# Kernel tuning notes

Hardware: AMD Instinct MI355X
Metric: run time of the kernel (lower is better)

The kernel has to match this reference:

```python
import jax, jax.numpy as jnp
import numpy as np

LRELU_ALPHA = 0.2
ACT_GAIN = float(np.sqrt(2.0))  # def_gain for 'lrelu' in StyleGAN2 bias_act


def setup_inputs() -> dict:
    key = jax.random.key(0)
    k_x, k_w, k_aw, k_wt = jax.random.split(key, 4)
    N, C_in, C_out, H, W, Wdim, K = 8, 256, 256, 128, 128, 512, 3
    x = jax.random.normal(k_x, (N, C_in, H, W), dtype=jnp.float32)
    w = jax.random.normal(k_w, (N, Wdim), dtype=jnp.float32)
    # FullyConnectedLayer params: weight ~ randn([out, in]) (lr_mult=1), bias_init=1
    affine_w = jax.random.normal(k_aw, (C_in, Wdim), dtype=jnp.float32)
    affine_b = jnp.ones((C_in,), dtype=jnp.float32)
    # Conv weight ~ randn, bias zeros
    weight = jax.random.normal(k_wt, (C_out, C_in, K, K), dtype=jnp.float32)
    bias = jnp.zeros((C_out,), dtype=jnp.float32)
    return {"x": x, "w": w, "affine_w": affine_w, "affine_b": affine_b,
            "weight": weight, "bias": bias}


def reference(x, w, affine_w, affine_b, weight, bias):
    N, C_in, H, W = x.shape
    C_out, _, K, _ = weight.shape
    # affine: runtime weight gain = 1/sqrt(in_features)
    wg = 1.0 / np.sqrt(affine_w.shape[1])
    styles = w @ (affine_w.T * wg) + affine_b                      # [N, C_in]
    # modulate: per-sample weights [N, C_out, C_in, K, K]
    ww = weight[None] * styles[:, None, :, None, None]
    # demodulate
    d = jax.lax.rsqrt(jnp.sum(ww * ww, axis=(2, 3, 4)) + 1e-8)     # [N, C_out]
    ww = ww * d[:, :, None, None, None]
    # fused per-sample conv via grouped conv (groups = N), flip_weight=True -> correlation
    x2 = x.reshape(1, N * C_in, H, W)
    wk = ww.reshape(N * C_out, C_in, K, K)
    pad = K // 2
    out = jax.lax.conv_general_dilated(
        x2, wk, window_strides=(1, 1), padding=((pad, pad), (pad, pad)),
        dimension_numbers=("NCHW", "OIHW", "NCHW"), feature_group_count=N)
    out = out.reshape(N, C_out, H, W)
    # bias_act: lrelu with def_gain sqrt(2), gain=1, no clamp; then sigmoid
    out = out + bias[None, :, None, None]
    out = jnp.where(out >= 0, out, LRELU_ALPHA * out) * ACT_GAIN
    return jax.nn.sigmoid(out)
```

## Files before the change

### kernel.cpp

```cpp
#include <hip/hip_runtime.h>
#include <hip/hip_bf16.h>

typedef __attribute__((ext_vector_type(8))) short bf16x8;
typedef __attribute__((ext_vector_type(4))) float f32x4;
typedef unsigned short ushort_t;

__device__ __forceinline__ void gload16(const void* g, void* l) {
  __builtin_amdgcn_global_load_lds(
      (const __attribute__((address_space(1))) void*)g,
      (__attribute__((address_space(3))) void*)l, 16, 0, 0);
}

__global__ void k_styles(const float* __restrict__ w, const float* __restrict__ aw,
                         const float* __restrict__ ab, float* __restrict__ styles) {
  int n = blockIdx.x;
  int ci = threadIdx.x;
  const float4* wr = (const float4*)(w + n * 512);
  const float4* ar = (const float4*)(aw + (size_t)ci * 512);
  float s = 0.f;
  #pragma unroll 4
  for (int j = 0; j < 128; j++) {
    float4 a = ar[j], b = wr[j];
    s += a.x * b.x + a.y * b.y + a.z * b.z + a.w * b.w;
  }
  styles[n * 256 + ci] = s * 0.044194173824159216f + ab[ci];
}

__global__ void k_modw(const float* __restrict__ weight, const float* __restrict__ styles,
                       ushort_t* __restrict__ wwg) {
  int id = blockIdx.x * 4 + (threadIdx.x >> 6);
  int l = threadIdx.x & 63;
  int n = id >> 8, co = id & 255;
  const float* wrow = weight + (size_t)co * 2304;
  const float* srow = styles + n * 256;
  float mv[36];
  float sum = 0.f;
  #pragma unroll
  for (int tap = 0; tap < 9; tap++) {
    #pragma unroll
    for (int cg = 0; cg < 4; cg++) {
      int ci = cg * 64 + l;
      float v = wrow[ci * 9 + tap] * srow[ci];
      mv[tap * 4 + cg] = v;
      sum += v * v;
    }
  }
  #pragma unroll
  for (int off = 32; off; off >>= 1) sum += __shfl_xor(sum, off, 64);
  float d = rsqrtf(sum + 1e-8f);
  #pragma unroll
  for (int tap = 0; tap < 9; tap++) {
    int kh = tap / 3, kw = tap % 3;
    #pragma unroll
    for (int cg = 0; cg < 4; cg++) {
      int ci = cg * 64 + l;
      float v = mv[tap * 4 + cg] * d;
      __hip_bfloat16 hb = __float2bfloat16(v);
      size_t oidx = ((((size_t)((n * 3 + kh) * 8) + (ci >> 5)) * 3 + kw) * 256 + co) * 32 + (ci & 31);
      wwg[oidx] = *reinterpret_cast<ushort_t*>(&hb);
    }
  }
}

__global__ void k_transpose(const float* __restrict__ x, ushort_t* __restrict__ xt) {
  int n = blockIdx.z, h = blockIdx.y;
  int wt = blockIdx.x & 1, ct = blockIdx.x >> 1;
  int w0 = wt * 64, ci0 = ct * 64;
  __shared__ float tile[64][65];
  int t = threadIdx.x;
  {
    int ci_l = t >> 2, wq = (t & 3) * 16;
    const float* src = x + (((size_t)(n * 256 + ci0 + ci_l) * 128 + h) * 128 + w0 + wq);
    #pragma unroll
    for (int j = 0; j < 4; j++) {
      float4 v = ((const float4*)src)[j];
      tile[ci_l][wq + j * 4 + 0] = v.x;
      tile[ci_l][wq + j * 4 + 1] = v.y;
      tile[ci_l][wq + j * 4 + 2] = v.z;
      tile[ci_l][wq + j * 4 + 3] = v.w;
    }
  }
  __syncthreads();
  {
    int w_l = t >> 2, cq = (t & 3) * 16;
    union { ushort_t u[16]; uint4 v[2]; } pk;
    #pragma unroll
    for (int j = 0; j < 16; j++) {
      __hip_bfloat16 hb = __float2bfloat16(tile[cq + j][w_l]);
      pk.u[j] = *reinterpret_cast<ushort_t*>(&hb);
    }
    size_t off = ((size_t)((n * 128 + h) * 128) + w0 + w_l) * 256 + ci0 + cq;
    uint4* dst = (uint4*)(xt + off);
    dst[0] = pk.v[0];
    dst[1] = pk.v[1];
  }
}

__global__ __launch_bounds__(256, 2) void k_conv(
    const ushort_t* __restrict__ xt, const ushort_t* __restrict__ wwg,
    const float* __restrict__ bias, float* __restrict__ out) {
  __shared__ __align__(16) char smem[24576 + 2 * 8448];
  char* sA = smem;
  char* sB = smem + 24576;

  const int cb = blockIdx.x;
  const int h0 = blockIdx.y * 2;
  const int n  = blockIdx.z;

  const int t = threadIdx.x;
  const int wave = t >> 6;
  const int l = t & 63;
  const int wr = wave >> 1, wc = wave & 1;
  const int c = l & 15, kg = l >> 4;

  f32x4 acc[4][8];
  #pragma unroll
  for (int i = 0; i < 4; i++)
    #pragma unroll
    for (int j = 0; j < 8; j++)
      acc[i][j] = (f32x4){0.f, 0.f, 0.f, 0.f};

  if (t < 64) {
    int buf = t >> 5;
    int r = t & 31;
    if (r < 16) {
      int rowsel = r >> 2;
      int row = (rowsel == 0) ? 0 : (128 + rowsel);
      *(f32x4*)(sB + buf * 8448 + row * 64 + (r & 3) * 16) = (f32x4){0.f, 0.f, 0.f, 0.f};
    }
  }

  const long long xtN = (long long)n * (128LL * 128 * 256);

  for (int kh = 0; kh < 3; kh++) {
    const int hsrc_w = h0 + wc + kh - 1;
    const bool valid = (hsrc_w >= 0) && (hsrc_w < 128);
    const char* gAkh = (const char*)(wwg + ((size_t)(n * 3 + kh)) * (8 * 3 * 256 * 32));
    for (int cc = 0; cc < 8; cc++) {
      __syncthreads();
      const char* gA = gAkh + (size_t)cc * (3 * 256 * 32 * 2);
      #pragma unroll
      for (int i = 0; i < 6; i++) {
        int G = i * 256 + t;
        int kw = G >> 9, r = G & 511;
        const char* gp = gA + kw * 16384 + cb * 8192 + r * 16;
        char* lp = sA + (i * 256 + wave * 64) * 16;
        gload16(gp, lp);
      }
      #pragma unroll
      for (int i = 0; i < 4; i++) {
        int G = i * 256 + t;
        int r = G & 511;
        int w = r >> 2, gg = r & 3;
        int buf = G >> 9;
        int hsrc = h0 + kh - 1 + buf;
        const char* gp = (const char*)xt +
            ((xtN + (long long)(hsrc * 128 + w) * 256 + cc * 32 + gg * 8) * 2);
        int B0 = i * 256 + wave * 64;
        char* lp = sB + (B0 >> 9) * 8448 + 64 + (B0 & 511) * 16;
        gload16(gp, lp);
      }
      asm volatile("s_waitcnt vmcnt(0)" ::: "memory");
      __syncthreads();
      if (valid) {
        const char* bBase = sB + wc * 8448;
        #pragma unroll
        for (int s = 0; s < 3; s++) {
          bf16x8 af[4];
          #pragma unroll
          for (int mi = 0; mi < 4; mi++)
            af[mi] = *(const bf16x8*)(sA + s * 8192 + (wr * 64 + mi * 16 + c) * 64 + kg * 16);
          bf16x8 bfr[8];
          #pragma unroll
          for (int ni = 0; ni < 8; ni++)
            bfr[ni] = *(const bf16x8*)(bBase + (ni * 16 + c + s) * 64 + kg * 16);
          #pragma unroll
          for (int mi = 0; mi < 4; mi++)
            #pragma unroll
            for (int ni = 0; ni < 8; ni++)
              acc[mi][ni] = __builtin_amdgcn_mfma_f32_16x16x32_bf16(af[mi], bfr[ni], acc[mi][ni], 0, 0, 0);
        }
      }
    }
  }

  const int hrow = h0 + wc;
  #pragma unroll
  for (int mi = 0; mi < 4; mi++) {
    #pragma unroll
    for (int r = 0; r < 4; r++) {
      int co = cb * 128 + wr * 64 + mi * 16 + kg * 4 + r;
      float bval = bias[co];
      #pragma unroll
      for (int ni = 0; ni < 8; ni++) {
        float v = acc[mi][ni][r] + bval;
        v = (v >= 0.f ? v : 0.2f * v) * 1.41421356237f;
        float o = 1.f / (1.f + __expf(-v));
        out[(((size_t)(n * 256 + co)) * 128 + hrow) * 128 + ni * 16 + c] = o;
      }
    }
  }
}

extern "C" void kernel_launch(void* const* d_in, const int* in_sizes, int n_in,
                              void* d_out, int out_size, void* d_ws, size_t ws_size,
                              hipStream_t stream) {
  const float* x      = (const float*)d_in[0];
  const float* w      = (const float*)d_in[1];
  const float* aw     = (const float*)d_in[2];
  const float* ab     = (const float*)d_in[3];
  const float* weight = (const float*)d_in[4];
  const float* bias   = (const float*)d_in[5];
  float* out = (float*)d_out;

  char* ws = (char*)d_ws;
  float*    styles = (float*)ws;
  ushort_t* wwg    = (ushort_t*)(ws + 8192);
  ushort_t* xt     = (ushort_t*)(ws + 8192 + 9437184);

  k_styles<<<8, 256, 0, stream>>>(w, aw, ab, styles);
  k_modw<<<512, 256, 0, stream>>>(weight, styles, wwg);
  k_transpose<<<dim3(8, 128, 8), 256, 0, stream>>>(x, xt);
  k_conv<<<dim3(2, 64, 8), 256, 0, stream>>>(xt, wwg, bias, out);
}
```

Before: 401.0 us.

## Parallelize styles and modw prep kernels, vectorize transpose, remap conv grid

The styles GEMV now runs one wave per output element with a shuffle reduction, so it launches 512 blocks instead of 8. The modulation kernel reads weight rows with coalesced loads staged through LDS instead of strided per-tap loads. The transpose writes its tile with float4 stores into a padded tile. The conv grid is flattened with batch index as the fastest-varying block id, which changes which blocks run concurrently and how they share weights and input in cache. The prep kernels are small next to the conv, so their effect on total time is limited, and the remap may help or hurt cache reuse.

```diff
diff --git a/kernel.cpp b/kernel.cpp
--- a/kernel.cpp
+++ b/kernel.cpp
@@ -13,48 +13,51 @@
 
 __global__ void k_styles(const float* __restrict__ w, const float* __restrict__ aw,
                          const float* __restrict__ ab, float* __restrict__ styles) {
-  int n = blockIdx.x;
-  int ci = threadIdx.x;
+  int wave = threadIdx.x >> 6, l = threadIdx.x & 63;
+  int id = blockIdx.x * 4 + wave;
+  int n = id >> 8, ci = id & 255;
+  const float4* ar = (const float4*)(aw + (size_t)ci * 512);
   const float4* wr = (const float4*)(w + n * 512);
-  const float4* ar = (const float4*)(aw + (size_t)ci * 512);
   float s = 0.f;
-  #pragma unroll 4
-  for (int j = 0; j < 128; j++) {
-    float4 a = ar[j], b = wr[j];
+  #pragma unroll
+  for (int j = 0; j < 2; j++) {
+    float4 a = ar[l * 2 + j], b = wr[l * 2 + j];
     s += a.x * b.x + a.y * b.y + a.z * b.z + a.w * b.w;
   }
-  styles[n * 256 + ci] = s * 0.044194173824159216f + ab[ci];
-}
-
-__global__ void k_modw(const float* __restrict__ weight, const float* __restrict__ styles,
-                       ushort_t* __restrict__ wwg) {
-  int id = blockIdx.x * 4 + (threadIdx.x >> 6);
-  int l = threadIdx.x & 63;
+  #pragma unroll
+  for (int off = 32; off; off >>= 1) s += __shfl_xor(s, off, 64);
+  if (l == 0) styles[n * 256 + ci] = s * 0.044194173824159216f + ab[ci];
+}
+
+__global__ __launch_bounds__(256) void k_modw(const float* __restrict__ weight,
+                                              const float* __restrict__ styles,
+                                              ushort_t* __restrict__ wwg) {
+  __shared__ float wl[4][2304];
+  __shared__ float s_sty[256];
+  int wave = threadIdx.x >> 6, l = threadIdx.x & 63;
+  int id = blockIdx.x * 4 + wave;
   int n = id >> 8, co = id & 255;
+  s_sty[threadIdx.x] = styles[(size_t)n * 256 + threadIdx.x];
+  __syncthreads();
   const float* wrow = weight + (size_t)co * 2304;
-  const float* srow = styles + n * 256;
-  float mv[36];
-  float sum = 0.f;
+  float sq = 0.f;
+  #pragma unroll
+  for (int i = 0; i < 36; i++) {
+    int idx = i * 64 + l;
+    float v = wrow[idx] * s_sty[idx / 9];
+    sq += v * v;
+    wl[wave][idx] = v;
+  }
+  #pragma unroll
+  for (int off = 32; off; off >>= 1) sq += __shfl_xor(sq, off, 64);
+  float d = rsqrtf(sq + 1e-8f);
   #pragma unroll
   for (int tap = 0; tap < 9; tap++) {
+    int kh = tap / 3, kw = tap % 3;
     #pragma unroll
     for (int cg = 0; cg < 4; cg++) {
       int ci = cg * 64 + l;
-      float v = wrow[ci * 9 + tap] * srow[ci];
-      mv[tap * 4 + cg] = v;
-      sum += v * v;
-    }
-  }
-  #pragma unroll
-  for (int off = 32; off; off >>= 1) sum += __shfl_xor(sum, off, 64);
-  float d = rsqrtf(sum + 1e-8f);
-  #pragma unroll
-  for (int tap = 0; tap < 9; tap++) {
-    int kh = tap / 3, kw = tap % 3;
-    #pragma unroll
-    for (int cg = 0; cg < 4; cg++) {
-      int ci = cg * 64 + l;
-      float v = mv[tap * 4 + cg] * d;
+      float v = wl[wave][ci * 9 + tap] * d;
       __hip_bfloat16 hb = __float2bfloat16(v);
       size_t oidx = ((((size_t)((n * 3 + kh) * 8) + (ci >> 5)) * 3 + kw) * 256 + co) * 32 + (ci & 31);
       wwg[oidx] = *reinterpret_cast<ushort_t*>(&hb);
@@ -66,19 +69,14 @@
   int n = blockIdx.z, h = blockIdx.y;
   int wt = blockIdx.x & 1, ct = blockIdx.x >> 1;
   int w0 = wt * 64, ci0 = ct * 64;
-  __shared__ float tile[64][65];
+  __shared__ float tile[64][68];
   int t = threadIdx.x;
   {
     int ci_l = t >> 2, wq = (t & 3) * 16;
     const float* src = x + (((size_t)(n * 256 + ci0 + ci_l) * 128 + h) * 128 + w0 + wq);
     #pragma unroll
-    for (int j = 0; j < 4; j++) {
-      float4 v = ((const float4*)src)[j];
-      tile[ci_l][wq + j * 4 + 0] = v.x;
-      tile[ci_l][wq + j * 4 + 1] = v.y;
-      tile[ci_l][wq + j * 4 + 2] = v.z;
-      tile[ci_l][wq + j * 4 + 3] = v.w;
-    }
+    for (int j = 0; j < 4; j++)
+      *(float4*)&tile[ci_l][wq + j * 4] = ((const float4*)src)[j];
   }
   __syncthreads();
   {
@@ -103,9 +101,11 @@
   char* sA = smem;
   char* sB = smem + 24576;
 
-  const int cb = blockIdx.x;
-  const int h0 = blockIdx.y * 2;
-  const int n  = blockIdx.z;
+  const int bid = blockIdx.x;
+  const int n  = bid & 7;
+  const int r  = bid >> 3;
+  const int cb = r & 1;
+  const int h0 = (r >> 1) * 2;
 
   const int t = threadIdx.x;
   const int wave = t >> 6;
@@ -122,11 +122,11 @@
 
   if (t < 64) {
     int buf = t >> 5;
-    int r = t & 31;
-    if (r < 16) {
-      int rowsel = r >> 2;
+    int rr = t & 31;
+    if (rr < 16) {
+      int rowsel = rr >> 2;
       int row = (rowsel == 0) ? 0 : (128 + rowsel);
-      *(f32x4*)(sB + buf * 8448 + row * 64 + (r & 3) * 16) = (f32x4){0.f, 0.f, 0.f, 0.f};
+      *(f32x4*)(sB + buf * 8448 + row * 64 + (rr & 3) * 16) = (f32x4){0.f, 0.f, 0.f, 0.f};
     }
   }
 
@@ -142,16 +142,16 @@
       #pragma unroll
       for (int i = 0; i < 6; i++) {
         int G = i * 256 + t;
-        int kw = G >> 9, r = G & 511;
-        const char* gp = gA + kw * 16384 + cb * 8192 + r * 16;
+        int kw = G >> 9, rr = G & 511;
+        const char* gp = gA + kw * 16384 + cb * 8192 + rr * 16;
         char* lp = sA + (i * 256 + wave * 64) * 16;
         gload16(gp, lp);
       }
       #pragma unroll
       for (int i = 0; i < 4; i++) {
         int G = i * 256 + t;
-        int r = G & 511;
-        int w = r >> 2, gg = r & 3;
+        int rr = G & 511;
+        int w = rr >> 2, gg = rr & 3;
         int buf = G >> 9;
         int hsrc = h0 + kh - 1 + buf;
         const char* gp = (const char*)xt +
@@ -188,12 +188,12 @@
   #pragma unroll
   for (int mi = 0; mi < 4; mi++) {
     #pragma unroll
-    for (int r = 0; r < 4; r++) {
-      int co = cb * 128 + wr * 64 + mi * 16 + kg * 4 + r;
+    for (int rr = 0; rr < 4; rr++) {
+      int co = cb * 128 + wr * 64 + mi * 16 + kg * 4 + rr;
       float bval = bias[co];
       #pragma unroll
       for (int ni = 0; ni < 8; ni++) {
-        float v = acc[mi][ni][r] + bval;
+        float v = acc[mi][ni][rr] + bval;
         v = (v >= 0.f ? v : 0.2f * v) * 1.41421356237f;
         float o = 1.f / (1.f + __expf(-v));
         out[(((size_t)(n * 256 + co)) * 128 + hrow) * 128 + ni * 16 + c] = o;
@@ -218,8 +218,8 @@
   ushort_t* wwg    = (ushort_t*)(ws + 8192);
   ushort_t* xt     = (ushort_t*)(ws + 8192 + 9437184);
 
-  k_styles<<<8, 256, 0, stream>>>(w, aw, ab, styles);
+  k_styles<<<512, 256, 0, stream>>>(w, aw, ab, styles);
   k_modw<<<512, 256, 0, stream>>>(weight, styles, wwg);
   k_transpose<<<dim3(8, 128, 8), 256, 0, stream>>>(x, xt);
-  k_conv<<<dim3(2, 64, 8), 256, 0, stream>>>(xt, wwg, bias, out);
-}
+  k_conv<<<1024, 256, 0, stream>>>(xt, wwg, bias, out);
+}
```

Result: faster. 377.2 us (-5.9%).
